# Performance work log

Measured on AMD Instinct MI355X. Metric: run time of the kernel, lower is better.

## Reference

```python
import jax, jax.numpy as jnp
import numpy as np

N1 = 10000; N2 = 10000; F_IN = 256
E_EDGES = 480000; P_PAIRS = 200000
HID = 128; H = 8; DH = 16; L = 2


def _segment_softmax(logits, seg, n):
    # softmax over edges sharing the same destination node (per head)
    m = jax.ops.segment_max(logits, seg, num_segments=n)
    m = jnp.where(jnp.isfinite(m), m, 0.0)
    e = jnp.exp(logits - m[seg])
    s = jax.ops.segment_sum(e, seg, num_segments=n)
    return e / (s[seg] + 1e-16)


def _attend(q_dst, k_src, v_src, src, dst, arel, mrel, prior, n_dst):
    # q_dst: [Nd,H,D]; k_src/v_src: [Ns,H,D]; arel/mrel: [H,D,D]; prior: [H]
    k = jnp.einsum('nhd,hde->nhe', k_src, arel)[src]   # [E,H,D]
    v = jnp.einsum('nhd,hde->nhe', v_src, mrel)[src]   # [E,H,D]
    logits = jnp.einsum('ehd,ehd->eh', q_dst[dst], k) * prior / jnp.sqrt(jnp.asarray(DH, q_dst.dtype))
    a = _segment_softmax(logits, dst, n_dst)           # [E,H]
    out = jax.ops.segment_sum(a[..., None] * v, dst, num_segments=n_dst)
    return out.reshape(n_dst, HID)


def _forward(x_n1, x_n2, Win1, bin1, Win2, bin2, Wk, bk, Wq, bq, Wv, bv, Wa, ba, skip, arel, mrel, prior, ei12, ei21, edge_index):
    proj = lambda x, W, b: (x @ W + b).reshape(-1, H, DH)
    h1 = jax.nn.relu(x_n1 @ Win1 + bin1)
    h2 = jax.nn.relu(x_n2 @ Win2 + bin2)
    feats1, feats2 = [], []
    for l in range(L):
        k1, q1, v1 = proj(h1, Wk[l, 0], bk[l, 0]), proj(h1, Wq[l, 0], bq[l, 0]), proj(h1, Wv[l, 0], bv[l, 0])
        k2, q2, v2 = proj(h2, Wk[l, 1], bk[l, 1]), proj(h2, Wq[l, 1], bq[l, 1]), proj(h2, Wv[l, 1], bv[l, 1])
        # edge type 0: n1 -> n2 (dst = n2); edge type 1: n2 -> n1 (dst = n1)
        agg2 = _attend(q2, k1, v1, ei12[0], ei12[1], arel[l, 0], mrel[l, 0], prior[l, 0], N2)
        agg1 = _attend(q1, k2, v2, ei21[0], ei21[1], arel[l, 1], mrel[l, 1], prior[l, 1], N1)
        o1 = jax.nn.gelu(agg1) @ Wa[l, 0] + ba[l, 0]
        o2 = jax.nn.gelu(agg2) @ Wa[l, 1] + ba[l, 1]
        s1 = jax.nn.sigmoid(skip[l, 0]); s2 = jax.nn.sigmoid(skip[l, 1])
        h1 = s1 * o1 + (1.0 - s1) * h1
        h2 = s2 * o2 + (1.0 - s2) * h2
        feats1.append(h1); feats2.append(h2)
    Em = jnp.concatenate(feats1, axis=1)   # [N1, HID*L]
    Ed = jnp.concatenate(feats2, axis=1)   # [N2, HID*L]
    # scores = Em @ Ed.T then gather at (m_index, d_index); computed as gathered dot
    # products (same math, avoids [N1,N2] materialization). Dropout in eval mode.
    preds = jnp.einsum('pc,pc->p', Em[edge_index[0]], Ed[edge_index[1]])[:, None]
    return preds


def setup_inputs():
    key = jax.random.key(0)
    ks = jax.random.split(key, 16)
    sc = 0.05
    inp = {}
    inp['x_n1'] = jax.random.normal(ks[0], (N1, F_IN), jnp.float32)
    inp['x_n2'] = jax.random.normal(ks[1], (N2, F_IN), jnp.float32)
    inp['ei12'] = jnp.stack([jax.random.randint(ks[2], (E_EDGES,), 0, N1),
                             jax.random.randint(ks[3], (E_EDGES,), 0, N2)])
    inp['ei21'] = jnp.stack([jax.random.randint(ks[4], (E_EDGES,), 0, N2),
                             jax.random.randint(ks[5], (E_EDGES,), 0, N1)])
    inp['edge_index'] = jnp.stack([jax.random.randint(ks[6], (P_PAIRS,), 0, N1),
                                   jax.random.randint(ks[7], (P_PAIRS,), 0, N2)])
    inp['Win1'] = jax.random.normal(ks[8], (F_IN, HID), jnp.float32) * sc
    inp['bin1'] = jnp.zeros((HID,), jnp.float32)
    inp['Win2'] = jax.random.normal(ks[9], (F_IN, HID), jnp.float32) * sc
    inp['bin2'] = jnp.zeros((HID,), jnp.float32)
    inp['Wk'] = jax.random.normal(ks[10], (L, 2, HID, HID), jnp.float32) * sc
    inp['bk'] = jnp.zeros((L, 2, HID), jnp.float32)
    inp['Wq'] = jax.random.normal(ks[11], (L, 2, HID, HID), jnp.float32) * sc
    inp['bq'] = jnp.zeros((L, 2, HID), jnp.float32)
    inp['Wv'] = jax.random.normal(ks[12], (L, 2, HID, HID), jnp.float32) * sc
    inp['bv'] = jnp.zeros((L, 2, HID), jnp.float32)
    inp['Wa'] = jax.random.normal(ks[13], (L, 2, HID, HID), jnp.float32) * sc
    inp['ba'] = jnp.zeros((L, 2, HID), jnp.float32)
    inp['skip'] = jnp.ones((L, 2), jnp.float32)
    inp['arel'] = jax.random.normal(ks[14], (L, 2, H, DH, DH), jnp.float32) * 0.25
    inp['mrel'] = jax.random.normal(ks[15], (L, 2, H, DH, DH), jnp.float32) * 0.25
    inp['prior'] = jnp.ones((L, 2, H), jnp.float32)
    return inp


def reference(x_n1, x_n2, ei12, ei21, edge_index, Win1, bin1, Win2, bin2, Wk, bk, Wq, bq, Wv, bv, Wa, ba, skip, arel, mrel, prior):
    return _forward(x_n1, x_n2, Win1, bin1, Win2, bin2, Wk, bk, Wq, bq, Wv, bv, Wa, ba, skip, arel, mrel, prior, ei12, ei21, edge_index)
```

## Files before the change

kernel.cpp:

```cpp
#include <hip/hip_runtime.h>
#include <math.h>

#define N1c 10000
#define N2c 10000
#define F_INc 256
#define Ec 480000
#define Pc 200000
#define Lc 2
#define NPART 32
#define NPc 313
#define NBLK 256

using short8 = __attribute__((ext_vector_type(8))) short;
using float4v = __attribute__((ext_vector_type(4))) float;
using floatx2 = __attribute__((ext_vector_type(2))) float;

__device__ __forceinline__ float gelu_f(float x) {
    const float k0 = 0.7978845608028654f;
    const float k1 = 0.044715f;
    float x3 = x * x * x;
    float t = tanhf(k0 * (x + k1 * x3));
    return 0.5f * x * (1.0f + t);
}

__device__ __forceinline__ float bf2f(unsigned short x) {
    union { unsigned int u; float f; } c;
    c.u = ((unsigned int)x) << 16;
    return c.f;
}
__device__ __forceinline__ unsigned short f2bf(float f) {
    union { float f; unsigned int u; } c;
    c.f = f;
    unsigned int u = c.u;
    unsigned int r = (u + 0x7FFFu + ((u >> 16) & 1u)) >> 16;
    return (unsigned short)r;
}
__device__ __forceinline__ unsigned char f2fp8(float v) {
    unsigned int p = __builtin_amdgcn_cvt_pk_fp8_f32(v, v, 0u, false);
    return (unsigned char)(p & 0xFF);
}

__global__ __launch_bounds__(256) void prep_kernel(
    const float* __restrict__ Wq, const float* __restrict__ bq,
    const float* __restrict__ Wk, const float* __restrict__ bk,
    const float* __restrict__ Wv, const float* __restrict__ bv,
    const float* __restrict__ arel, const float* __restrict__ mrel,
    const float* __restrict__ prior,
    const float* __restrict__ Win1, const float* __restrict__ Win2,
    const float* __restrict__ Wa,
    short* __restrict__ Wqkvt, float* __restrict__ bqkv,
    short* __restrict__ Wint1, short* __restrict__ Wint2, short* __restrict__ Wat)
{
    int id = blockIdx.x * 256 + threadIdx.x;
    if (id < 196608) {
        int lt = id / 49152;
        int r = id - lt * 49152;
        int col = r >> 7, c = r & 127;
        short* Wout = Wqkvt + (size_t)lt * 384 * 128;
        float* bout = bqkv + lt * 384;
        if (col < 128) {
            Wout[col * 128 + c] = (short)f2bf(Wq[lt * 16384 + c * 128 + col]);
            if (c == 0) bout[col] = bq[lt * 128 + col];
            return;
        }
        int which = (col < 256) ? 0 : 1;
        int he = col - (which ? 256 : 128);
        int h = he >> 4, e = he & 15;
        const float* W = (which == 0 ? Wk : Wv) + lt * 16384;
        const float* b = (which == 0 ? bk : bv) + lt * 128;
        const float* R = (which == 0 ? arel : mrel) + lt * 2048;
        float sc = (which == 0) ? prior[lt * 8 + h] * 0.25f : 1.0f;
        float acc = 0.f;
        #pragma unroll
        for (int d = 0; d < 16; d++)
            acc += W[c * 128 + h * 16 + d] * R[(h * 16 + d) * 16 + e];
        Wout[col * 128 + c] = (short)f2bf(acc * sc);
        if (c == 0) {
            float bacc = 0.f;
            #pragma unroll
            for (int d = 0; d < 16; d++)
                bacc += b[h * 16 + d] * R[(h * 16 + d) * 16 + e];
            bout[col] = bacc * sc;
        }
    } else {
        int wid = id - 196608;
        if (wid < 65536) {
            int y = wid >> 15;
            int id2 = wid & 32767;
            int n = id2 >> 8, k = id2 & 255;
            const float* W = y ? Win2 : Win1;
            short* O = y ? Wint2 : Wint1;
            O[n * 256 + k] = (short)f2bf(W[k * 128 + n]);
        } else {
            int wid2 = wid - 65536;
            int lt = wid2 >> 14;
            int id2 = wid2 & 16383;
            int n = id2 >> 7, k = id2 & 127;
            Wat[lt * 16384 + n * 128 + k] = (short)f2bf(Wa[lt * 16384 + k * 128 + n]);
        }
    }
}

__global__ __launch_bounds__(256) void count_bins_kernel(
    const int* __restrict__ ei12, const int* __restrict__ ei21, const int* __restrict__ eidx,
    int* __restrict__ cntmat)
{
    int blk = blockIdx.x, z = blockIdx.y, t = threadIdx.x;
    const int* key; int E;
    if (z == 0)      { key = ei12 + Ec; E = Ec; }
    else if (z == 1) { key = ei21 + Ec; E = Ec; }
    else             { key = eidx;      E = Pc; }
    int chunk = (E + NBLK - 1) / NBLK;
    int start = blk * chunk;
    int stop = min(start + chunk, E);
    __shared__ int cnt[NPART];
    if (t < NPART) cnt[t] = 0;
    __syncthreads();
    for (int e = start + t; e < stop; e += 256)
        atomicAdd(&cnt[key[e] / NPc], 1);
    __syncthreads();
    if (t < NPART) cntmat[z * (NPART * NBLK) + t * NBLK + blk] = cnt[t];
}

__global__ __launch_bounds__(256) void scan_bins_kernel(
    const int* __restrict__ cntmat, int* __restrict__ offmat)
{
    int z = blockIdx.x, t = threadIdx.x;
    const int* c = cntmat + z * (NPART * NBLK);
    int* o = offmat + z * (NPART * NBLK);
    int loc[32];
    int base = t * 32;
    int s = 0;
    #pragma unroll
    for (int j = 0; j < 32; j++) { loc[j] = s; s += c[base + j]; }
    __shared__ int ws[256];
    ws[t] = s;
    __syncthreads();
    for (int off = 1; off < 256; off <<= 1) {
        int v = (t >= off) ? ws[t - off] : 0;
        __syncthreads();
        ws[t] += v;
        __syncthreads();
    }
    int excl = t ? ws[t - 1] : 0;
    #pragma unroll
    for (int j = 0; j < 32; j++) o[base + j] = excl + loc[j];
}

__global__ __launch_bounds__(256) void binwrite_kernel(
    const int* __restrict__ ei12, const int* __restrict__ ei21, const int* __restrict__ eidx,
    const int* __restrict__ offmat,
    unsigned int* __restrict__ stg12, unsigned int* __restrict__ stg21,
    unsigned int* __restrict__ stgm)
{
    int blk = blockIdx.x, z = blockIdx.y, t = threadIdx.x;
    const int* key; const int* pay; int E; unsigned int* stg;
    if (z == 0)      { key = ei12 + Ec; pay = ei12; E = Ec; stg = stg12; }
    else if (z == 1) { key = ei21 + Ec; pay = ei21; E = Ec; stg = stg21; }
    else             { key = eidx;      pay = nullptr; E = Pc; stg = stgm; }
    int chunk = (E + NBLK - 1) / NBLK;
    int start = blk * chunk;
    int stop = min(start + chunk, E);
    const int* om = offmat + z * (NPART * NBLK);
    __shared__ int fill[NPART];
    __shared__ int obase[NPART];
    if (t < NPART) { fill[t] = 0; obase[t] = om[t * NBLK + blk]; }
    __syncthreads();
    for (int e = start + t; e < stop; e += 256) {
        unsigned int k = (unsigned int)key[e];
        int p = (int)(k / NPc);
        int r = atomicAdd(&fill[p], 1);
        unsigned int pk = (z == 2) ? ((k << 18) | (unsigned int)e)
                                   : ((k << 14) | (unsigned int)pay[e]);
        stg[obase[p] + r] = pk;
    }
}

__global__ __launch_bounds__(256) void build_csr_kernel(
    const int* __restrict__ offmat,
    const unsigned int* __restrict__ stg12, const unsigned int* __restrict__ stg21,
    const unsigned int* __restrict__ stgm,
    int* __restrict__ rp12, int* __restrict__ rp21, int* __restrict__ rpm,
    int* __restrict__ es12, int* __restrict__ es21, int* __restrict__ ps)
{
    int p = blockIdx.x, z = blockIdx.y, t = threadIdx.x;
    const unsigned int* stg; int* rowptr; int* out; int E;
    if (z == 0)      { stg = stg12; rowptr = rp12; out = es12; E = Ec; }
    else if (z == 1) { stg = stg21; rowptr = rp21; out = es21; E = Ec; }
    else             { stg = stgm;  rowptr = rpm;  out = ps;   E = Pc; }
    int ksh = (z == 2) ? 18 : 14;
    unsigned int pmask = (z == 2) ? 0x3FFFFu : 0x3FFFu;
    const int* om = offmat + z * (NPART * NBLK);
    int base = om[p * NBLK];
    int next = (p == NPART - 1) ? E : om[(p + 1) * NBLK];
    int cntP = next - base;
    int lo = p * NPc;
    int hi = min(lo + NPc, 10000);

    __shared__ int hist[512];
    __shared__ int fill[NPc];
    hist[t] = 0; hist[t + 256] = 0;
    __syncthreads();
    for (int i = t; i < cntP; i += 256)
        atomicAdd(&hist[(int)(stg[base + i] >> ksh) - lo], 1);
    __syncthreads();
    for (int off = 1; off < 512; off <<= 1) {
        int i0 = t, i1 = t + 256;
        int v0 = (i0 >= off) ? hist[i0 - off] : 0;
        int v1 = (i1 >= off) ? hist[i1 - off] : 0;
        __syncthreads();
        hist[i0] += v0; hist[i1] += v1;
        __syncthreads();
    }
    for (int i = t; i < NPc; i += 256) {
        int excl = i ? hist[i - 1] : 0;
        fill[i] = excl;
        if (lo + i < hi) rowptr[lo + i] = base + excl;
    }
    if (p == NPART - 1 && t == 0) rowptr[10000] = E;
    __syncthreads();
    for (int i = t; i < cntP; i += 256) {
        unsigned int pk = stg[base + i];
        int r = atomicAdd(&fill[(int)(pk >> ksh) - lo], 1);
        out[base + r] = (int)(pk & pmask);
    }
}

template<int A_GELU, int OUT_RELU, int SKIP, int PACKQKV, int ABF, int KT>
__global__ __launch_bounds__(256) void gemm_mfma(
    const void* __restrict__ A0v, const void* __restrict__ A1v, int ldA,
    const short* __restrict__ Wt0, const short* __restrict__ Wt1,
    const float* __restrict__ b0, const float* __restrict__ b1,
    unsigned short* __restrict__ C0, unsigned short* __restrict__ C1, int ldC,
    unsigned char* __restrict__ K8o0, unsigned char* __restrict__ K8o1,
    unsigned short* __restrict__ Vb0, unsigned short* __restrict__ Vb1,
    int M,
    const float* __restrict__ sk0, const float* __restrict__ sk1,
    const unsigned short* __restrict__ H0, const unsigned short* __restrict__ H1, int ldH)
{
    int z = blockIdx.z;
    const void* Av = z ? A1v : A0v;
    const short* Wt = z ? Wt1 : Wt0;
    const float* bias = z ? b1 : b0;
    unsigned short* C = z ? C1 : C0;
    unsigned char* K8o = z ? K8o1 : K8o0;
    unsigned short* Vbo = z ? Vb1 : Vb0;
    const float* skipv = z ? sk1 : sk0;
    const unsigned short* Hold = z ? H1 : H0;

    __shared__ short Alds[64 * 40];
    __shared__ short Blds[64 * 40];

    int tid = threadIdx.x;
    int w = tid >> 6;
    int l = tid & 63;
    int mBase = blockIdx.x * 64;
    int nBase = blockIdx.y * 64;

    int srow = tid >> 2;
    int koct = tid & 3;

    float4v acc[4];
    #pragma unroll
    for (int i = 0; i < 4; i++) acc[i] = (float4v){0.f, 0.f, 0.f, 0.f};

    int arow = mBase + srow;
    const short* Wptr = Wt + (size_t)(nBase + srow) * KT + koct * 8;

    int fl = l & 15;
    int fo = (l >> 4) * 8;

    #pragma unroll
    for (int k0 = 0; k0 < KT; k0 += 32) {
        uint4 raw;
        if (ABF) {
            const unsigned short* Ab = (const unsigned short*)Av;
            raw = make_uint4(0u, 0u, 0u, 0u);
            if (arow < M) raw = *(const uint4*)(Ab + (size_t)arow * ldA + k0 + koct * 8);
            if (A_GELU) {
                unsigned int wd[4] = {raw.x, raw.y, raw.z, raw.w};
                #pragma unroll
                for (int i = 0; i < 4; i++) {
                    float lo = gelu_f(bf2f((unsigned short)(wd[i] & 0xFFFFu)));
                    float hi = gelu_f(bf2f((unsigned short)(wd[i] >> 16)));
                    wd[i] = (unsigned int)f2bf(lo) | ((unsigned int)f2bf(hi) << 16);
                }
                raw = make_uint4(wd[0], wd[1], wd[2], wd[3]);
            }
        } else {
            const float* Af = (const float*)Av;
            float av[8];
            if (arow < M) {
                const float4* p = (const float4*)(Af + (size_t)arow * ldA + k0 + koct * 8);
                float4 f0 = p[0], f1 = p[1];
                av[0]=f0.x; av[1]=f0.y; av[2]=f0.z; av[3]=f0.w;
                av[4]=f1.x; av[5]=f1.y; av[6]=f1.z; av[7]=f1.w;
            } else {
                #pragma unroll
                for (int i = 0; i < 8; i++) av[i] = 0.f;
            }
            unsigned int pk[4];
            #pragma unroll
            for (int i = 0; i < 4; i++)
                pk[i] = (unsigned int)f2bf(av[2*i]) | ((unsigned int)f2bf(av[2*i+1]) << 16);
            raw = make_uint4(pk[0], pk[1], pk[2], pk[3]);
        }
        *(uint4*)&Alds[srow * 40 + koct * 8] = raw;
        *(uint4*)&Blds[srow * 40 + koct * 8] = *(const uint4*)(Wptr + k0);
        __syncthreads();

        short8 bfr = *(const short8*)&Blds[(w * 16 + fl) * 40 + fo];
        #pragma unroll
        for (int msub = 0; msub < 4; msub++) {
            short8 afr = *(const short8*)&Alds[(msub * 16 + fl) * 40 + fo];
            acc[msub] = __builtin_amdgcn_mfma_f32_16x16x32_bf16(afr, bfr, acc[msub], 0, 0, 0);
        }
        __syncthreads();
    }

    float sig = 0.f;
    if (SKIP) sig = 1.f / (1.f + __expf(-skipv[0]));
    int col = nBase + w * 16 + fl;
    float bcol = bias[col];
    int rbase = mBase + ((l >> 4) * 4);
    #pragma unroll
    for (int msub = 0; msub < 4; msub++) {
        #pragma unroll
        for (int r = 0; r < 4; r++) {
            int row = rbase + msub * 16 + r;
            if (row >= M) continue;
            float v = acc[msub][r] + bcol;
            if (OUT_RELU) v = fmaxf(v, 0.f);
            if (SKIP) v = sig * v + (1.f - sig) * bf2f(Hold[(size_t)row * ldH + col]);
            if (PACKQKV) {
                if (col < 128) C[(size_t)row * ldC + col] = f2bf(v);
                else if (col < 256) K8o[(size_t)row * 128 + (col - 128)] = f2fp8(v);
                else Vbo[(size_t)row * 128 + (col - 256)] = f2bf(v);
            } else {
                C[(size_t)row * ldC + col] = f2bf(v);
            }
        }
    }
}

__global__ __launch_bounds__(128) void attend_kernel(
    const unsigned short* __restrict__ Qb, const unsigned char* __restrict__ K8,
    const unsigned short* __restrict__ Vb,
    const int* __restrict__ rp, const int* __restrict__ es,
    unsigned short* __restrict__ outb)
{
    int n = blockIdx.x * 8 + (threadIdx.x >> 4);
    int ln = threadIdx.x & 15;

    float q[8];
    {
        const ushort4* qp = (const ushort4*)(Qb + (size_t)n * 128 + 8 * ln);
        ushort4 qa = qp[0], qc = qp[1];
        q[0]=bf2f(qa.x); q[1]=bf2f(qa.y); q[2]=bf2f(qa.z); q[3]=bf2f(qa.w);
        q[4]=bf2f(qc.x); q[5]=bf2f(qc.y); q[6]=bf2f(qc.z); q[7]=bf2f(qc.w);
    }
    int beg = rp[n], end = rp[n + 1];
    float s = 0.f;
    float acc[8];
    #pragma unroll
    for (int c = 0; c < 8; c++) acc[c] = 0.f;

    auto edge_kv = [&](int e, float* kd, float* vd) {
        const unsigned char* kr = K8 + (size_t)e * 128 + 8 * ln;
        uint2 kw = *(const uint2*)kr;
        floatx2 k01 = __builtin_amdgcn_cvt_pk_f32_fp8(kw.x, false);
        floatx2 k23 = __builtin_amdgcn_cvt_pk_f32_fp8(kw.x, true);
        floatx2 k45 = __builtin_amdgcn_cvt_pk_f32_fp8(kw.y, false);
        floatx2 k67 = __builtin_amdgcn_cvt_pk_f32_fp8(kw.y, true);
        kd[0]=k01[0]; kd[1]=k01[1]; kd[2]=k23[0]; kd[3]=k23[1];
        kd[4]=k45[0]; kd[5]=k45[1]; kd[6]=k67[0]; kd[7]=k67[1];
        const ushort4* vr = (const ushort4*)(Vb + (size_t)e * 128 + 8 * ln);
        ushort4 v0 = vr[0], v1 = vr[1];
        vd[0]=bf2f(v0.x); vd[1]=bf2f(v0.y); vd[2]=bf2f(v0.z); vd[3]=bf2f(v0.w);
        vd[4]=bf2f(v1.x); vd[5]=bf2f(v1.y); vd[6]=bf2f(v1.z); vd[7]=bf2f(v1.w);
    };
    auto dot8 = [&](const float* kd) {
        float p = q[0]*kd[0] + q[1]*kd[1] + q[2]*kd[2] + q[3]*kd[3]
                + q[4]*kd[4] + q[5]*kd[5] + q[6]*kd[6] + q[7]*kd[7];
        p += __shfl_xor(p, 1, 2);
        return p;
    };

    int i = beg;
    int pre = min(end, (beg + 3) & ~3);
    for (; i < pre; i++) {
        float kd[8], vd[8];
        edge_kv(es[i], kd, vd);
        float x = __expf(dot8(kd));
        s += x;
        #pragma unroll
        for (int c = 0; c < 8; c++) acc[c] += x * vd[c];
    }
    for (; i + 4 <= end; i += 4) {
        int4 e = *(const int4*)&es[i];
        float k0[8], v0[8], k1[8], v1[8], k2[8], v2[8], k3[8], v3[8];
        edge_kv(e.x, k0, v0);
        edge_kv(e.y, k1, v1);
        edge_kv(e.z, k2, v2);
        edge_kv(e.w, k3, v3);
        float x0 = __expf(dot8(k0));
        float x1 = __expf(dot8(k1));
        float x2 = __expf(dot8(k2));
        float x3 = __expf(dot8(k3));
        s += (x0 + x1) + (x2 + x3);
        #pragma unroll
        for (int c = 0; c < 8; c++)
            acc[c] += x0 * v0[c] + x1 * v1[c] + x2 * v2[c] + x3 * v3[c];
    }
    for (; i < end; i++) {
        float kd[8], vd[8];
        edge_kv(es[i], kd, vd);
        float x = __expf(dot8(kd));
        s += x;
        #pragma unroll
        for (int c = 0; c < 8; c++) acc[c] += x * vd[c];
    }

    float inv = 1.f / (s + 1e-16f);
    unsigned int w0 = (unsigned int)f2bf(acc[0]*inv) | ((unsigned int)f2bf(acc[1]*inv) << 16);
    unsigned int w1 = (unsigned int)f2bf(acc[2]*inv) | ((unsigned int)f2bf(acc[3]*inv) << 16);
    unsigned int w2 = (unsigned int)f2bf(acc[4]*inv) | ((unsigned int)f2bf(acc[5]*inv) << 16);
    unsigned int w3 = (unsigned int)f2bf(acc[6]*inv) | ((unsigned int)f2bf(acc[7]*inv) << 16);
    *(uint4*)(outb + (size_t)n * 128 + 8 * ln) = make_uint4(w0, w1, w2, w3);
}

__global__ __launch_bounds__(256) void pred_kernel(
    const unsigned short* __restrict__ Emb, const unsigned short* __restrict__ Edb,
    const int* __restrict__ eidx,
    const int* __restrict__ rpm, const int* __restrict__ porder,
    float* __restrict__ out)
{
    int m = blockIdx.x * 4 + (threadIdx.x >> 6);
    int lane = threadIdx.x & 63;
    int beg = rpm[m], end = rpm[m + 1];
    if (beg == end) return;
    ushort4 au = *(const ushort4*)(Emb + (size_t)m * 256 + 4 * lane);
    float4 a = make_float4(bf2f(au.x), bf2f(au.y), bf2f(au.z), bf2f(au.w));
    int i = beg;
    for (; i + 2 <= end; i += 2) {
        int p0 = porder[i], p1 = porder[i + 1];
        int d0 = eidx[Pc + p0], d1 = eidx[Pc + p1];
        ushort4 u0 = *(const ushort4*)(Edb + (size_t)d0 * 256 + 4 * lane);
        ushort4 u1 = *(const ushort4*)(Edb + (size_t)d1 * 256 + 4 * lane);
        float s0 = a.x*bf2f(u0.x) + a.y*bf2f(u0.y) + a.z*bf2f(u0.z) + a.w*bf2f(u0.w);
        float s1 = a.x*bf2f(u1.x) + a.y*bf2f(u1.y) + a.z*bf2f(u1.z) + a.w*bf2f(u1.w);
        #pragma unroll
        for (int o = 1; o < 64; o <<= 1) { s0 += __shfl_xor(s0, o); s1 += __shfl_xor(s1, o); }
        if (lane == 0) { out[p0] = s0; out[p1] = s1; }
    }
    if (i < end) {
        int p0 = porder[i];
        int d0 = eidx[Pc + p0];
        ushort4 u0 = *(const ushort4*)(Edb + (size_t)d0 * 256 + 4 * lane);
        float s0 = a.x*bf2f(u0.x) + a.y*bf2f(u0.y) + a.z*bf2f(u0.z) + a.w*bf2f(u0.w);
        #pragma unroll
        for (int o = 1; o < 64; o <<= 1) s0 += __shfl_xor(s0, o);
        if (lane == 0) out[p0] = s0;
    }
}

extern "C" void kernel_launch(void* const* d_in, const int* in_sizes, int n_in,
                              void* d_out, int out_size, void* d_ws, size_t ws_size,
                              hipStream_t stream)
{
    const float* x1   = (const float*)d_in[0];
    const float* x2   = (const float*)d_in[1];
    const int*   ei12 = (const int*)d_in[2];
    const int*   ei21 = (const int*)d_in[3];
    const int*   eidx = (const int*)d_in[4];
    const float* Win1 = (const float*)d_in[5];
    const float* bin1 = (const float*)d_in[6];
    const float* Win2 = (const float*)d_in[7];
    const float* bin2 = (const float*)d_in[8];
    const float* Wk   = (const float*)d_in[9];
    const float* bk   = (const float*)d_in[10];
    const float* Wq   = (const float*)d_in[11];
    const float* bq   = (const float*)d_in[12];
    const float* Wv   = (const float*)d_in[13];
    const float* bv   = (const float*)d_in[14];
    const float* Wa   = (const float*)d_in[15];
    const float* ba   = (const float*)d_in[16];
    const float* skip = (const float*)d_in[17];
    const float* arel = (const float*)d_in[18];
    const float* mrel = (const float*)d_in[19];
    const float* prior= (const float*)d_in[20];

    char* ws = (char*)d_ws;
    size_t off = 0;
    auto allocB = [&](size_t bytes) { void* p = ws + off; off += (bytes + 15) & ~15ull; return p; };
    auto allocF = [&](size_t n) { return (float*)allocB(n * 4); };
    auto allocI = [&](size_t n) { return (int*)allocB(n * 4); };
    auto allocS = [&](size_t n) { return (short*)allocB(n * 2); };
    auto allocU = [&](size_t n) { return (unsigned short*)allocB(n * 2); };

    unsigned short* h1b  = allocU((size_t)N1c * 128);
    unsigned short* h2b  = allocU((size_t)N2c * 128);
    unsigned short* Qb1  = allocU((size_t)N1c * 128);
    unsigned short* Qb2  = allocU((size_t)N2c * 128);
    unsigned char*  K81  = (unsigned char*)allocB((size_t)N1c * 128);
    unsigned char*  K82  = (unsigned char*)allocB((size_t)N2c * 128);
    unsigned short* Vb1  = allocU((size_t)N1c * 128);
    unsigned short* Vb2  = allocU((size_t)N2c * 128);
    unsigned short* agg1 = allocU((size_t)N1c * 128);
    unsigned short* agg2 = allocU((size_t)N2c * 128);
    unsigned short* Emb  = allocU((size_t)N1c * 256);
    unsigned short* Edb  = allocU((size_t)N2c * 256);
    float* bqkv  = allocF(4 * 384);
    short* Wqkvt = allocS(4 * 384 * 128);
    short* Wint1 = allocS(128 * 256);
    short* Wint2 = allocS(128 * 256);
    short* Wat   = allocS(4 * 128 * 128);
    int* rp12  = allocI(N2c + 1);
    int* rp21  = allocI(N1c + 1);
    int* rpm   = allocI(N1c + 1);
    int* es12  = allocI(Ec);
    int* es21  = allocI(Ec);
    int* ps    = allocI(Pc);
    int* cntmat = allocI(3 * NPART * NBLK);
    int* offmat = allocI(3 * NPART * NBLK);
    unsigned int* stg12 = (unsigned int*)allocB((size_t)Ec * 4);
    unsigned int* stg21 = (unsigned int*)allocB((size_t)Ec * 4);
    unsigned int* stgm  = (unsigned int*)allocB((size_t)Pc * 4);

    prep_kernel<<<1280, 256, 0, stream>>>(
        Wq, bq, Wk, bk, Wv, bv, arel, mrel, prior,
        Win1, Win2, Wa, Wqkvt, bqkv, Wint1, Wint2, Wat);

    count_bins_kernel<<<dim3(NBLK, 3), 256, 0, stream>>>(ei12, ei21, eidx, cntmat);
    scan_bins_kernel<<<3, 256, 0, stream>>>(cntmat, offmat);
    binwrite_kernel<<<dim3(NBLK, 3), 256, 0, stream>>>(ei12, ei21, eidx, offmat,
                                                       stg12, stg21, stgm);
    build_csr_kernel<<<dim3(NPART, 3), 256, 0, stream>>>(offmat, stg12, stg21, stgm,
                                                         rp12, rp21, rpm, es12, es21, ps);

    const int MB = (N1c + 63) / 64;
    gemm_mfma<0, 1, 0, 0, 0, 256><<<dim3(MB, 2, 2), 256, 0, stream>>>(
        x1, x2, F_INc, Wint1, Wint2, bin1, bin2, h1b, h2b, 128,
        nullptr, nullptr, nullptr, nullptr,
        N1c, nullptr, nullptr, nullptr, nullptr, 0);

    for (int l = 0; l < Lc; l++) {
        const unsigned short* A1 = (l == 0) ? h1b : Emb;  int ld1 = (l == 0) ? 128 : 256;
        const unsigned short* A2 = (l == 0) ? h2b : Edb;
        int lt0 = l * 2 + 0, lt1 = l * 2 + 1;
        gemm_mfma<0, 0, 0, 1, 1, 128><<<dim3(MB, 6, 2), 256, 0, stream>>>(
            A1, A2, ld1,
            Wqkvt + (size_t)lt0 * 49152, Wqkvt + (size_t)lt1 * 49152,
            bqkv + lt0 * 384, bqkv + lt1 * 384,
            Qb1, Qb2, 128,
            K81, K82, Vb1, Vb2,
            N1c, nullptr, nullptr, nullptr, nullptr, 0);
        attend_kernel<<<N2c / 8, 128, 0, stream>>>(Qb2, K81, Vb1, rp12, es12, agg2);
        attend_kernel<<<N1c / 8, 128, 0, stream>>>(Qb1, K82, Vb2, rp21, es21, agg1);
        gemm_mfma<1, 0, 1, 0, 1, 128><<<dim3(MB, 2, 2), 256, 0, stream>>>(
            agg1, agg2, 128,
            Wat + (size_t)lt0 * 16384, Wat + (size_t)lt1 * 16384,
            ba + lt0 * 128, ba + lt1 * 128,
            Emb + l * 128, Edb + l * 128, 256,
            nullptr, nullptr, nullptr, nullptr,
            N1c,
            skip + lt0, skip + lt1,
            A1, A2, ld1);
    }

    pred_kernel<<<N1c / 4, 256, 0, stream>>>(Emb, Edb, eidx, rpm, ps, (float*)d_out);
}
```

Before: 357.5 us.

## Store V in fp8 and unroll attention gathers by eight edges

The V projection is now written as fp8 instead of bf16, which halves the bytes gathered per edge for values in the attention kernel. The attention loop also issues all K/V loads for eight edges before decoding and accumulating, to increase memory-level parallelism. This lowers precision of the value vectors, which risks accuracy, and the wider batch raises register pressure.

```diff
diff --git a/kernel.cpp b/kernel.cpp
--- a/kernel.cpp
+++ b/kernel.cpp
@@ -233,7 +233,7 @@
     const float* __restrict__ b0, const float* __restrict__ b1,
     unsigned short* __restrict__ C0, unsigned short* __restrict__ C1, int ldC,
     unsigned char* __restrict__ K8o0, unsigned char* __restrict__ K8o1,
-    unsigned short* __restrict__ Vb0, unsigned short* __restrict__ Vb1,
+    unsigned char* __restrict__ V8o0, unsigned char* __restrict__ V8o1,
     int M,
     const float* __restrict__ sk0, const float* __restrict__ sk1,
     const unsigned short* __restrict__ H0, const unsigned short* __restrict__ H1, int ldH)
@@ -244,7 +244,7 @@
     const float* bias = z ? b1 : b0;
     unsigned short* C = z ? C1 : C0;
     unsigned char* K8o = z ? K8o1 : K8o0;
-    unsigned short* Vbo = z ? Vb1 : Vb0;
+    unsigned char* V8o = z ? V8o1 : V8o0;
     const float* skipv = z ? sk1 : sk0;
     const unsigned short* Hold = z ? H1 : H0;
 
@@ -335,7 +335,7 @@
             if (PACKQKV) {
                 if (col < 128) C[(size_t)row * ldC + col] = f2bf(v);
                 else if (col < 256) K8o[(size_t)row * 128 + (col - 128)] = f2fp8(v);
-                else Vbo[(size_t)row * 128 + (col - 256)] = f2bf(v);
+                else V8o[(size_t)row * 128 + (col - 256)] = f2fp8(v);
             } else {
                 C[(size_t)row * ldC + col] = f2bf(v);
             }
@@ -345,7 +345,7 @@
 
 __global__ __launch_bounds__(128) void attend_kernel(
     const unsigned short* __restrict__ Qb, const unsigned char* __restrict__ K8,
-    const unsigned short* __restrict__ Vb,
+    const unsigned char* __restrict__ V8,
     const int* __restrict__ rp, const int* __restrict__ es,
     unsigned short* __restrict__ outb)
 {
@@ -365,60 +365,60 @@
     #pragma unroll
     for (int c = 0; c < 8; c++) acc[c] = 0.f;
 
-    auto edge_kv = [&](int e, float* kd, float* vd) {
-        const unsigned char* kr = K8 + (size_t)e * 128 + 8 * ln;
-        uint2 kw = *(const uint2*)kr;
-        floatx2 k01 = __builtin_amdgcn_cvt_pk_f32_fp8(kw.x, false);
-        floatx2 k23 = __builtin_amdgcn_cvt_pk_f32_fp8(kw.x, true);
-        floatx2 k45 = __builtin_amdgcn_cvt_pk_f32_fp8(kw.y, false);
-        floatx2 k67 = __builtin_amdgcn_cvt_pk_f32_fp8(kw.y, true);
-        kd[0]=k01[0]; kd[1]=k01[1]; kd[2]=k23[0]; kd[3]=k23[1];
-        kd[4]=k45[0]; kd[5]=k45[1]; kd[6]=k67[0]; kd[7]=k67[1];
-        const ushort4* vr = (const ushort4*)(Vb + (size_t)e * 128 + 8 * ln);
-        ushort4 v0 = vr[0], v1 = vr[1];
-        vd[0]=bf2f(v0.x); vd[1]=bf2f(v0.y); vd[2]=bf2f(v0.z); vd[3]=bf2f(v0.w);
-        vd[4]=bf2f(v1.x); vd[5]=bf2f(v1.y); vd[6]=bf2f(v1.z); vd[7]=bf2f(v1.w);
+    auto dec8 = [&](uint2 w, float* d) {
+        floatx2 a0 = __builtin_amdgcn_cvt_pk_f32_fp8(w.x, false);
+        floatx2 a1 = __builtin_amdgcn_cvt_pk_f32_fp8(w.x, true);
+        floatx2 a2 = __builtin_amdgcn_cvt_pk_f32_fp8(w.y, false);
+        floatx2 a3 = __builtin_amdgcn_cvt_pk_f32_fp8(w.y, true);
+        d[0]=a0[0]; d[1]=a0[1]; d[2]=a1[0]; d[3]=a1[1];
+        d[4]=a2[0]; d[5]=a2[1]; d[6]=a3[0]; d[7]=a3[1];
     };
-    auto dot8 = [&](const float* kd) {
+    auto proc1 = [&](uint2 kw, uint2 vw) {
+        float kd[8], vd[8];
+        dec8(kw, kd);
         float p = q[0]*kd[0] + q[1]*kd[1] + q[2]*kd[2] + q[3]*kd[3]
                 + q[4]*kd[4] + q[5]*kd[5] + q[6]*kd[6] + q[7]*kd[7];
         p += __shfl_xor(p, 1, 2);
-        return p;
+        float x = __expf(p);
+        s += x;
+        dec8(vw, vd);
+        #pragma unroll
+        for (int c = 0; c < 8; c++) acc[c] += x * vd[c];
     };
+    auto ldk = [&](int e) { return *(const uint2*)(K8 + (size_t)e * 128 + 8 * ln); };
+    auto ldv = [&](int e) { return *(const uint2*)(V8 + (size_t)e * 128 + 8 * ln); };
 
     int i = beg;
     int pre = min(end, (beg + 3) & ~3);
     for (; i < pre; i++) {
-        float kd[8], vd[8];
-        edge_kv(es[i], kd, vd);
-        float x = __expf(dot8(kd));
-        s += x;
-        #pragma unroll
-        for (int c = 0; c < 8; c++) acc[c] += x * vd[c];
+        int e = es[i];
+        proc1(ldk(e), ldv(e));
+    }
+    for (; i + 8 <= end; i += 8) {
+        int4 ea = *(const int4*)&es[i];
+        int4 eb = *(const int4*)&es[i + 4];
+        uint2 kw0 = ldk(ea.x), vw0 = ldv(ea.x);
+        uint2 kw1 = ldk(ea.y), vw1 = ldv(ea.y);
+        uint2 kw2 = ldk(ea.z), vw2 = ldv(ea.z);
+        uint2 kw3 = ldk(ea.w), vw3 = ldv(ea.w);
+        uint2 kw4 = ldk(eb.x), vw4 = ldv(eb.x);
+        uint2 kw5 = ldk(eb.y), vw5 = ldv(eb.y);
+        uint2 kw6 = ldk(eb.z), vw6 = ldv(eb.z);
+        uint2 kw7 = ldk(eb.w), vw7 = ldv(eb.w);
+        proc1(kw0, vw0); proc1(kw1, vw1); proc1(kw2, vw2); proc1(kw3, vw3);
+        proc1(kw4, vw4); proc1(kw5, vw5); proc1(kw6, vw6); proc1(kw7, vw7);
     }
     for (; i + 4 <= end; i += 4) {
-        int4 e = *(const int4*)&es[i];
-        float k0[8], v0[8], k1[8], v1[8], k2[8], v2[8], k3[8], v3[8];
-        edge_kv(e.x, k0, v0);
-        edge_kv(e.y, k1, v1);
-        edge_kv(e.z, k2, v2);
-        edge_kv(e.w, k3, v3);
-        float x0 = __expf(dot8(k0));
-        float x1 = __expf(dot8(k1));
-        float x2 = __expf(dot8(k2));
-        float x3 = __expf(dot8(k3));
-        s += (x0 + x1) + (x2 + x3);
-        #pragma unroll
-        for (int c = 0; c < 8; c++)
-            acc[c] += x0 * v0[c] + x1 * v1[c] + x2 * v2[c] + x3 * v3[c];
+        int4 ea = *(const int4*)&es[i];
+        uint2 kw0 = ldk(ea.x), vw0 = ldv(ea.x);
+        uint2 kw1 = ldk(ea.y), vw1 = ldv(ea.y);
+        uint2 kw2 = ldk(ea.z), vw2 = ldv(ea.z);
+        uint2 kw3 = ldk(ea.w), vw3 = ldv(ea.w);
+        proc1(kw0, vw0); proc1(kw1, vw1); proc1(kw2, vw2); proc1(kw3, vw3);
     }
     for (; i < end; i++) {
-        float kd[8], vd[8];
-        edge_kv(es[i], kd, vd);
-        float x = __expf(dot8(kd));
-        s += x;
-        #pragma unroll
-        for (int c = 0; c < 8; c++) acc[c] += x * vd[c];
+        int e = es[i];
+        proc1(ldk(e), ldv(e));
     }
 
     float inv = 1.f / (s + 1e-16f);
@@ -504,8 +504,8 @@
     unsigned short* Qb2  = allocU((size_t)N2c * 128);
     unsigned char*  K81  = (unsigned char*)allocB((size_t)N1c * 128);
     unsigned char*  K82  = (unsigned char*)allocB((size_t)N2c * 128);
-    unsigned short* Vb1  = allocU((size_t)N1c * 128);
-    unsigned short* Vb2  = allocU((size_t)N2c * 128);
+    unsigned char*  V81  = (unsigned char*)allocB((size_t)N1c * 128);
+    unsigned char*  V82  = (unsigned char*)allocB((size_t)N2c * 128);
     unsigned short* agg1 = allocU((size_t)N1c * 128);
     unsigned short* agg2 = allocU((size_t)N2c * 128);
     unsigned short* Emb  = allocU((size_t)N1c * 256);
@@ -553,10 +553,10 @@
             Wqkvt + (size_t)lt0 * 49152, Wqkvt + (size_t)lt1 * 49152,
             bqkv + lt0 * 384, bqkv + lt1 * 384,
             Qb1, Qb2, 128,
-            K81, K82, Vb1, Vb2,
+            K81, K82, V81, V82,
             N1c, nullptr, nullptr, nullptr, nullptr, 0);
-        attend_kernel<<<N2c / 8, 128, 0, stream>>>(Qb2, K81, Vb1, rp12, es12, agg2);
-        attend_kernel<<<N1c / 8, 128, 0, stream>>>(Qb1, K82, Vb2, rp21, es21, agg1);
+        attend_kernel<<<N2c / 8, 128, 0, stream>>>(Qb2, K81, V81, rp12, es12, agg2);
+        attend_kernel<<<N1c / 8, 128, 0, stream>>>(Qb1, K82, V82, rp21, es21, agg1);
         gemm_mfma<1, 0, 1, 0, 1, 128><<<dim3(MB, 2, 2), 256, 0, stream>>>(
             agg1, agg2, 128,
             Wat + (size_t)lt0 * 16384, Wat + (size_t)lt1 * 16384,
```

New measurement: 339.2 us. 1.05x faster.
